# Performance work log

Hardware: AMD Instinct MI355X
Metric: run time of the kernel (lower is better)

## Reference

```python
import jax, jax.numpy as jnp
import numpy as np

# Dimensions (see shape_source)
L = 1024   # episode_len (memory slots)
B = 64     # batch (parallel envs)
K = 512    # key_size
V = 512    # value_size
H = 8      # num_head
MEMB = 256 # memory_state_embedding
SDIM = 512 # state_dim
HID = 512  # hidden width of all 2-layer encoders
RIMQ = 512 # rim_query_size
LAT = K - MEMB  # task_inference_latent dim


def setup_inputs() -> dict:
    key = jax.random.key(0)
    ks = jax.random.split(key, 16)
    w = lambda k, shape: (jax.random.normal(k, shape, jnp.float32) * 0.02)
    return {
        "state": jax.random.normal(ks[0], (B, SDIM), jnp.float32),
        "task_inference_latent": jax.random.normal(ks[1], (B, LAT), jnp.float32),
        "keys": jax.random.normal(ks[2], (L, B, K), jnp.float32),
        "vals": jax.random.normal(ks[3], (L, B, V), jnp.float32),
        "rpe_mod": jax.random.uniform(ks[4], (L, B, 1), jnp.float32),
        "step": jnp.maximum(jax.random.randint(ks[5], (B,), 0, L), 1),
        "W_state": w(ks[6], (SDIM, MEMB)), "b_state": jnp.zeros((MEMB,), jnp.float32),
        "Wcq1": w(ks[7], (K, HID)), "bcq1": jnp.zeros((HID,), jnp.float32),
        "Wcq2": w(ks[8], (HID, K)), "bcq2": jnp.zeros((K,), jnp.float32),
        "Wq": w(ks[9], (K, H * K)), "bq": jnp.zeros((H * K,), jnp.float32),
        "Wagg": w(ks[10], (H * V, V)), "bagg": jnp.zeros((V,), jnp.float32),
        "Wrk1": w(ks[11], (V, HID)), "brk1": jnp.zeros((HID,), jnp.float32),
        "Wrk2": w(ks[12], (HID, RIMQ)), "brk2": jnp.zeros((RIMQ,), jnp.float32),
        "Wrv1": w(ks[13], (V, HID)), "brv1": jnp.zeros((HID,), jnp.float32),
        "Wrv2": w(ks[14], (HID, V)), "brv2": jnp.zeros((V,), jnp.float32),
    }


def reference(state, task_inference_latent, keys, vals, rpe_mod, step,
              W_state, b_state, Wcq1, bcq1, Wcq2, bcq2, Wq, bq, Wagg, bagg,
              Wrk1, brk1, Wrk2, brk2, Wrv1, brv1, Wrv2, brv2):
    # DND.read (exploration branch), vectorized over the batch loop.
    se = state @ W_state + b_state                         # state_encoder: [B, MEMB]
    q = jnp.concatenate([se, task_inference_latent], -1)   # [B, K]
    # concat_query_encoder: stacked Linears with NO nonlinearity (faithful to source)
    q = (q @ Wcq1 + bcq1) @ Wcq2 + bcq2                    # [B, K]
    q = (q @ Wq + bq).reshape(B, H, K)                     # multi-head queries

    mk = keys * rpe_mod                                    # RPE-modulated keys [L, B, K]
    scores = jnp.einsum('lbk,bhk->blh', mk, q) / jnp.sqrt(jnp.float32(K))  # [B, L, H]
    valid = jnp.arange(L)[None, :] < step[:, None]         # [B, L] only slots < step[i]
    scores = jnp.where(valid[:, :, None], scores, jnp.float32(-1e30))
    prob = jax.nn.softmax(scores, axis=1) * valid[:, :, None].astype(scores.dtype)

    result = jnp.einsum('blh,lbv->bhv', prob, vals).reshape(B, H * V)
    result = (result @ Wagg + bagg)[:, None, :]            # value_aggregator -> [B, 1, V]
    out_key = (result @ Wrk1 + brk1) @ Wrk2 + brk2         # read_memory_to_key  [B, 1, RIMQ]
    out_val = (result @ Wrv1 + brv1) @ Wrv2 + brv2         # read_memory_to_value [B, 1, V]
    return out_key, out_val
```

## Files before the change

### kernel.cpp

```cpp
#include <hip/hip_runtime.h>
#include <math.h>

#define F4(p)  (*reinterpret_cast<float4*>(p))
#define CF4(p) (*reinterpret_cast<const float4*>(p))

#define NCHUNK 32

__device__ __forceinline__ void gemm_core(
    const float* __restrict__ Asrc, const float* __restrict__ inbias,
    const float* __restrict__ til,
    int NS, int srcld, int kc, int k0,
    const float* __restrict__ W, int ldw, int n0,
    const float* __restrict__ obias, float* __restrict__ Pout, int ldo)
{
    __shared__ float As[16*64], Ws[16*64];
    const int t = threadIdx.x;
    const int tx = t & 15, ty = t >> 4;
    const int row = t >> 2, kq = (t & 3) * 4;
    const int wrow = t >> 4, wcol = (t & 15) * 4;
    float acc[4][4] = {};
    for (int kk = 0; kk < kc; kk += 16) {
        const int kg = k0 + kk + kq;
        float4 av;
        if (til && kg >= 256) {
            av = CF4(&til[row*256 + (kg - 256)]);
        } else {
            av = {0.f, 0.f, 0.f, 0.f};
            if (inbias) av = CF4(&inbias[kg]);
            for (int s = 0; s < NS; ++s) {
                float4 v = CF4(&Asrc[(size_t)(s*64 + row)*srcld + kg]);
                av.x += v.x; av.y += v.y; av.z += v.z; av.w += v.w;
            }
        }
        As[(kq+0)*64+row] = av.x; As[(kq+1)*64+row] = av.y;
        As[(kq+2)*64+row] = av.z; As[(kq+3)*64+row] = av.w;
        F4(&Ws[wrow*64 + wcol]) = CF4(&W[(size_t)(k0 + kk + wrow)*ldw + n0 + wcol]);
        __syncthreads();
        #pragma unroll
        for (int k = 0; k < 16; ++k) {
            float4 a4 = CF4(&As[k*64 + ty*4]);
            float4 w4 = CF4(&Ws[k*64 + tx*4]);
            float a[4] = {a4.x, a4.y, a4.z, a4.w};
            float w[4] = {w4.x, w4.y, w4.z, w4.w};
            #pragma unroll
            for (int i = 0; i < 4; ++i)
                #pragma unroll
                for (int j = 0; j < 4; ++j)
                    acc[i][j] += a[i] * w[j];
        }
        __syncthreads();
    }
    #pragma unroll
    for (int i = 0; i < 4; ++i) {
        float4 o = {acc[i][0], acc[i][1], acc[i][2], acc[i][3]};
        if (obias) {
            float4 ob = CF4(&obias[n0 + tx*4]);
            o.x += ob.x; o.y += ob.y; o.z += ob.z; o.w += ob.w;
        }
        F4(&Pout[(size_t)(ty*4 + i)*ldo + n0 + tx*4]) = o;
    }
}

__global__ __launch_bounds__(256) void k_q1(
    const float* __restrict__ state, const float* __restrict__ W_state,
    float* __restrict__ P1)
{
    const int nt = blockIdx.x, ks = blockIdx.y;
    gemm_core(state, nullptr, nullptr, 1, 512, 64, ks*64,
              W_state, 256, nt*64, nullptr, P1 + (size_t)ks*64*256, 256);
}

__global__ __launch_bounds__(256) void k_q2(
    const float* __restrict__ P1, const float* __restrict__ b_state,
    const float* __restrict__ til, const float* __restrict__ Wcq1,
    float* __restrict__ P2)
{
    const int nt = blockIdx.x, ks = blockIdx.y;
    gemm_core(P1, b_state, til, 8, 256, 64, ks*64,
              Wcq1, 512, nt*64, nullptr, P2 + (size_t)ks*64*512, 512);
}

__global__ __launch_bounds__(256) void k_q3(
    const float* __restrict__ P2, const float* __restrict__ bcq1,
    const float* __restrict__ Wcq2, float* __restrict__ P3)
{
    const int nt = blockIdx.x, ks = blockIdx.y;
    gemm_core(P2, bcq1, nullptr, 8, 512, 64, ks*64,
              Wcq2, 512, nt*64, nullptr, P3 + (size_t)ks*64*512, 512);
}

__global__ __launch_bounds__(256) void k_qh(
    const float* __restrict__ P3, const float* __restrict__ bcq2,
    const float* __restrict__ Wq, float* __restrict__ P4)
{
    const int nt = blockIdx.x, ks = blockIdx.y;
    gemm_core(P3, bcq2, nullptr, 8, 512, 128, ks*128,
              Wq, 4096, nt*64, nullptr, P4 + (size_t)ks*64*4096, 4096);
}

__global__ __launch_bounds__(256) void k_qsum(
    const float* __restrict__ P4, const float* __restrict__ bq,
    float* __restrict__ qh)
{
    const int b = blockIdx.x, t = threadIdx.x;
    #pragma unroll
    for (int j = 0; j < 4; ++j) {
        int f = t + j*256;
        float4 v = CF4(&bq[f*4]);
        #pragma unroll
        for (int s = 0; s < 4; ++s) {
            float4 u = CF4(&P4[(size_t)(s*64 + b)*4096 + f*4]);
            v.x += u.x; v.y += u.y; v.z += u.z; v.w += u.w;
        }
        F4(&qh[(size_t)b*4096 + f*4]) = v;
    }
}

__global__ __launch_bounds__(256) void k_fa(
    const float* __restrict__ keys, const float* __restrict__ rpe,
    const float* __restrict__ qh, const float* __restrict__ vals,
    const int* __restrict__ step,
    float* __restrict__ Facc, float* __restrict__ Fms)
{
    __shared__ float s_q[4096];
    __shared__ float s_sc[64*8];
    __shared__ float red[256];
    __shared__ float s_m[8];
    const int b = blockIdx.y, lc = blockIdx.x;
    const int sb = step[b];
    const int l0 = (lc * sb) / NCHUNK;
    const int l1 = ((lc + 1) * sb) / NCHUNK;
    const int nl = l1 - l0;
    const int t = threadIdx.x;
    float* facc_out = Facc + ((size_t)(lc*64) + b)*4096;
    if (nl <= 0) {
        float4 z = {0.f, 0.f, 0.f, 0.f};
        for (int i = t; i < 1024; i += 256) F4(&facc_out[i*4]) = z;
        if (t < 8) {
            size_t o = ((size_t)(lc*64 + b)*8 + t)*2;
            Fms[o] = -1e30f; Fms[o+1] = 0.f;
        }
        return;
    }
    for (int i = t; i < 1024; i += 256)
        F4(&s_q[i*4]) = CF4(&qh[(size_t)b*4096 + i*4]);
    __syncthreads();
    const int lane = t & 63, w = t >> 6;
    float qr[8][8];
    #pragma unroll
    for (int h = 0; h < 8; ++h) {
        float4 x = CF4(&s_q[h*512 + lane*8]);
        float4 y = CF4(&s_q[h*512 + lane*8 + 4]);
        qr[h][0]=x.x; qr[h][1]=x.y; qr[h][2]=x.z; qr[h][3]=x.w;
        qr[h][4]=y.x; qr[h][5]=y.y; qr[h][6]=y.z; qr[h][7]=y.w;
    }
    const float inv_sqrtK = 0.04419417382415922f;
    const bool p0 = lane & 1, p1 = lane & 2, p2 = lane & 4;
    const size_t kstride = (size_t)4*64*512;
    const float* kp = keys + ((size_t)(l0 + w)*64 + b)*512 + lane*8;
    float4 k0x, k0y, k1x, k1y;
    if (w < nl)     { k0x = CF4(kp);           k0y = CF4(kp + 4); }
    if (w + 4 < nl) { k1x = CF4(kp + kstride); k1y = CF4(kp + kstride + 4); }
    for (int il = w; il < nl; il += 4) {
        float kv[8] = {k0x.x,k0x.y,k0x.z,k0x.w, k0y.x,k0y.y,k0y.z,k0y.w};
        k0x = k1x; k0y = k1y;
        if (il + 8 < nl) { k1x = CF4(kp + 2*kstride); k1y = CF4(kp + 2*kstride + 4); }
        kp += kstride;
        float pr[8] = {};
        #pragma unroll
        for (int h = 0; h < 8; ++h)
            #pragma unroll
            for (int j = 0; j < 8; ++j)
                pr[h] += kv[j] * qr[h][j];
        float w4[4], x2[2], y;
        #pragma unroll
        for (int i = 0; i < 4; ++i) {
            float keep = p0 ? pr[2*i+1] : pr[2*i];
            float send = p0 ? pr[2*i]   : pr[2*i+1];
            w4[i] = keep + __shfl_xor(send, 1);
        }
        #pragma unroll
        for (int i = 0; i < 2; ++i) {
            float keep = p1 ? w4[2*i+1] : w4[2*i];
            float send = p1 ? w4[2*i]   : w4[2*i+1];
            x2[i] = keep + __shfl_xor(send, 2);
        }
        {
            float keep = p2 ? x2[1] : x2[0];
            float send = p2 ? x2[0] : x2[1];
            y = keep + __shfl_xor(send, 4);
        }
        y += __shfl_xor(y, 8);
        y += __shfl_xor(y, 16);
        y += __shfl_xor(y, 32);
        if (lane < 8)
            s_sc[il*8 + lane] = y * rpe[(l0 + il)*64 + b] * inv_sqrtK;
    }
    __syncthreads();
    const int h = t & 7, g = t >> 3;
    float m = -1e30f;
    for (int l = g; l < nl; l += 32) m = fmaxf(m, s_sc[l*8 + h]);
    red[g*8 + h] = m;
    __syncthreads();
    #pragma unroll
    for (int s = 16; s; s >>= 1) {
        if (g < s) red[g*8+h] = fmaxf(red[g*8+h], red[(g+s)*8+h]);
        __syncthreads();
    }
    if (t < 8) s_m[t] = red[t];
    __syncthreads();
    float mh = s_m[h], s_acc = 0.f;
    for (int l = g; l < nl; l += 32) {
        float e = __expf(s_sc[l*8 + h] - mh);
        s_sc[l*8 + h] = e;
        s_acc += e;
    }
    red[g*8 + h] = s_acc;
    __syncthreads();
    #pragma unroll
    for (int s = 16; s; s >>= 1) {
        if (g < s) red[g*8+h] += red[(g+s)*8+h];
        __syncthreads();
    }
    if (t < 8) {
        size_t o = ((size_t)(lc*64 + b)*8 + t)*2;
        Fms[o] = s_m[t]; Fms[o+1] = red[t];
    }
    const int par = t >> 7, c = t & 127;
    float4 acc[8] = {};
    const size_t vstride = (size_t)2*64*512;
    const float* vp = vals + ((size_t)(l0 + par)*64 + b)*512 + c*4;
    float4 v0, v1, v2;
    if (par < nl)     v0 = CF4(vp);
    if (par + 2 < nl) v1 = CF4(vp + vstride);
    if (par + 4 < nl) v2 = CF4(vp + 2*vstride);
    for (int il = par; il < nl; il += 2) {
        float4 pa = CF4(&s_sc[il*8]);
        float4 pb = CF4(&s_sc[il*8 + 4]);
        acc[0].x += pa.x*v0.x; acc[0].y += pa.x*v0.y; acc[0].z += pa.x*v0.z; acc[0].w += pa.x*v0.w;
        acc[1].x += pa.y*v0.x; acc[1].y += pa.y*v0.y; acc[1].z += pa.y*v0.z; acc[1].w += pa.y*v0.w;
        acc[2].x += pa.z*v0.x; acc[2].y += pa.z*v0.y; acc[2].z += pa.z*v0.z; acc[2].w += pa.z*v0.w;
        acc[3].x += pa.w*v0.x; acc[3].y += pa.w*v0.y; acc[3].z += pa.w*v0.z; acc[3].w += pa.w*v0.w;
        acc[4].x += pb.x*v0.x; acc[4].y += pb.x*v0.y; acc[4].z += pb.x*v0.z; acc[4].w += pb.x*v0.w;
        acc[5].x += pb.y*v0.x; acc[5].y += pb.y*v0.y; acc[5].z += pb.y*v0.z; acc[5].w += pb.y*v0.w;
        acc[6].x += pb.z*v0.x; acc[6].y += pb.z*v0.y; acc[6].z += pb.z*v0.z; acc[6].w += pb.z*v0.w;
        acc[7].x += pb.w*v0.x; acc[7].y += pb.w*v0.y; acc[7].z += pb.w*v0.z; acc[7].w += pb.w*v0.w;
        v0 = v1; v1 = v2;
        if (il + 6 < nl) v2 = CF4(vp + 3*vstride);
        vp += vstride;
    }
    __syncthreads();
    if (par == 1) {
        #pragma unroll
        for (int hh = 0; hh < 8; ++hh)
            F4(&s_q[(c*8 + hh)*4]) = acc[hh];
    }
    __syncthreads();
    if (par == 0) {
        #pragma unroll
        for (int hh = 0; hh < 8; ++hh) {
            float4 o = CF4(&s_q[(c*8 + hh)*4]);
            o.x += acc[hh].x; o.y += acc[hh].y; o.z += acc[hh].z; o.w += acc[hh].w;
            F4(&facc_out[hh*512 + c*4]) = o;
        }
    }
}

__global__ __launch_bounds__(256) void k_comb(
    const float* __restrict__ Facc, const float* __restrict__ Fms,
    float* __restrict__ res)
{
    __shared__ float wgt[NCHUNK*8];
    const int b = blockIdx.x, t = threadIdx.x;
    if (t < 8) {
        float mm[NCHUNK], ss[NCHUNK], e[NCHUNK];
        float M = -1e30f;
        #pragma unroll
        for (int i = 0; i < NCHUNK; ++i) {
            size_t o = ((size_t)(i*64 + b)*8 + t)*2;
            mm[i] = Fms[o]; ss[i] = Fms[o+1];
            M = fmaxf(M, mm[i]);
        }
        float D = 0.f;
        #pragma unroll
        for (int i = 0; i < NCHUNK; ++i) { e[i] = __expf(mm[i] - M); D += e[i]*ss[i]; }
        float invD = 1.f / D;
        #pragma unroll
        for (int i = 0; i < NCHUNK; ++i) wgt[i*8 + t] = e[i] * invD;
    }
    __syncthreads();
    #pragma unroll
    for (int j = 0; j < 4; ++j) {
        int f = t + j*256;
        int h = f >> 7;
        float4 a = {0.f, 0.f, 0.f, 0.f};
        #pragma unroll
        for (int i = 0; i < NCHUNK; ++i) {
            float wi = wgt[i*8 + h];
            float4 v = CF4(&Facc[((size_t)(i*64) + b)*4096 + f*4]);
            a.x += wi*v.x; a.y += wi*v.y; a.z += wi*v.z; a.w += wi*v.w;
        }
        F4(&res[(size_t)b*4096 + f*4]) = a;
    }
}

__global__ __launch_bounds__(256) void k_agg(
    const float* __restrict__ res, const float* __restrict__ Wagg,
    float* __restrict__ P5)
{
    const int nt = blockIdx.x, ks = blockIdx.y;
    gemm_core(res, nullptr, nullptr, 1, 4096, 128, ks*128,
              Wagg, 512, nt*64, nullptr, P5 + (size_t)ks*64*512, 512);
}

__global__ __launch_bounds__(256) void k_rkv1(
    const float* __restrict__ P5, const float* __restrict__ bagg,
    const float* __restrict__ Wrk1, const float* __restrict__ Wrv1,
    float* __restrict__ P6)
{
    const int nt = blockIdx.x, ks = blockIdx.y, z = blockIdx.z;
    gemm_core(P5, bagg, nullptr, 32, 512, 128, ks*128,
              z ? Wrv1 : Wrk1, 512, nt*64,
              nullptr, P6 + (size_t)(z*4 + ks)*64*512, 512);
}

__global__ __launch_bounds__(256) void k_rkv2(
    const float* __restrict__ P6,
    const float* __restrict__ brk1, const float* __restrict__ brv1,
    const float* __restrict__ Wrk2, const float* __restrict__ Wrv2,
    const float* __restrict__ brk2, const float* __restrict__ brv2,
    float* __restrict__ out)
{
    const int nt = blockIdx.x, z = blockIdx.z;
    gemm_core(P6 + (size_t)z*4*64*512, z ? brv1 : brk1, nullptr, 4, 512, 512, 0,
              z ? Wrv2 : Wrk2, 512, nt*64,
              z ? brv2 : brk2, out + (size_t)z*64*512, 512);
}

extern "C" void kernel_launch(void* const* d_in, const int* in_sizes, int n_in,
                              void* d_out, int out_size, void* d_ws, size_t ws_size,
                              hipStream_t stream) {
    const float* state   = (const float*)d_in[0];
    const float* til     = (const float*)d_in[1];
    const float* keys    = (const float*)d_in[2];
    const float* vals    = (const float*)d_in[3];
    const float* rpe     = (const float*)d_in[4];
    const int*   step    = (const int*)d_in[5];
    const float* W_state = (const float*)d_in[6];
    const float* b_state = (const float*)d_in[7];
    const float* Wcq1 = (const float*)d_in[8];
    const float* bcq1 = (const float*)d_in[9];
    const float* Wcq2 = (const float*)d_in[10];
    const float* bcq2 = (const float*)d_in[11];
    const float* Wq   = (const float*)d_in[12];
    const float* bq   = (const float*)d_in[13];
    const float* Wagg = (const float*)d_in[14];
    const float* bagg = (const float*)d_in[15];
    const float* Wrk1 = (const float*)d_in[16];
    const float* brk1 = (const float*)d_in[17];
    const float* Wrk2 = (const float*)d_in[18];
    const float* brk2 = (const float*)d_in[19];
    const float* Wrv1 = (const float*)d_in[20];
    const float* brv1 = (const float*)d_in[21];
    const float* Wrv2 = (const float*)d_in[22];
    const float* brv2 = (const float*)d_in[23];
    float* out = (float*)d_out;
    float* ws  = (float*)d_ws;

    float* P1   = ws;
    float* P2   = ws + 131072;
    float* P3   = ws + 393216;
    float* P4   = ws + 655360;
    float* qh   = ws + 1703936;
    float* Facc = ws + 1966080;
    float* Fms  = ws + 10354688;
    float* res  = ws + 10387456;
    float* P5   = ws;
    float* P6   = ws + 1048576;

    k_q1  <<<dim3(4,8),   256, 0, stream>>>(state, W_state, P1);
    k_q2  <<<dim3(8,8),   256, 0, stream>>>(P1, b_state, til, Wcq1, P2);
    k_q3  <<<dim3(8,8),   256, 0, stream>>>(P2, bcq1, Wcq2, P3);
    k_qh  <<<dim3(64,4),  256, 0, stream>>>(P3, bcq2, Wq, P4);
    k_qsum<<<64, 256, 0, stream>>>(P4, bq, qh);
    k_fa  <<<dim3(NCHUNK,64), 256, 0, stream>>>(keys, rpe, qh, vals, step, Facc, Fms);
    k_comb<<<64, 256, 0, stream>>>(Facc, Fms, res);
    k_agg <<<dim3(8,32),  256, 0, stream>>>(res, Wagg, P5);
    k_rkv1<<<dim3(8,4,2), 256, 0, stream>>>(P5, bagg, Wrk1, Wrv1, P6);
    k_rkv2<<<dim3(8,1,2), 256, 0, stream>>>(P6, brk1, brv1, Wrk2, Wrv2,
                                            brk2, brv2, out);
}
```

Baseline: 169.4 us.

## Stage keys and values through double-buffered LDS tiles in attention kernel

The attention kernel now loads keys and values cooperatively, four rows at a time, into double-buffered shared-memory tiles with register prefetch. Queries are read from LDS inside the loop instead of being held in 64 registers per thread. This frees registers so launch_bounds can request 4 blocks per unit, and the chunk count is halved to 16 with workspace offsets adjusted to match. The trade is two barriers per tile, extra LDS traffic, and less L-parallelism per batch row.

```diff
diff --git a/kernel.cpp b/kernel.cpp
--- a/kernel.cpp
+++ b/kernel.cpp
@@ -4,7 +4,7 @@
 #define F4(p)  (*reinterpret_cast<float4*>(p))
 #define CF4(p) (*reinterpret_cast<const float4*>(p))
 
-#define NCHUNK 32
+#define NCHUNK 16
 
 __device__ __forceinline__ void gemm_core(
     const float* __restrict__ Asrc, const float* __restrict__ inbias,
@@ -116,14 +116,16 @@
     }
 }
 
-__global__ __launch_bounds__(256) void k_fa(
+__global__ __launch_bounds__(256, 4) void k_fa(
     const float* __restrict__ keys, const float* __restrict__ rpe,
     const float* __restrict__ qh, const float* __restrict__ vals,
     const int* __restrict__ step,
     float* __restrict__ Facc, float* __restrict__ Fms)
 {
     __shared__ float s_q[4096];
+    __shared__ float s_kt[2][2048];
     __shared__ float s_sc[64*8];
+    __shared__ float s_rpe[64];
     __shared__ float red[256];
     __shared__ float s_m[8];
     const int b = blockIdx.y, lc = blockIdx.x;
@@ -142,61 +144,80 @@
         }
         return;
     }
-    for (int i = t; i < 1024; i += 256)
-        F4(&s_q[i*4]) = CF4(&qh[(size_t)b*4096 + i*4]);
-    __syncthreads();
+    const int ntile = (nl + 3) >> 2;
+    const int j0 = t, j1 = t + 256;
+    const int r0 = j0 >> 7, c0 = (j0 & 127) * 4;
+    const int r1 = j1 >> 7, c1 = (j1 & 127) * 4;
+    const float inv_sqrtK = 0.04419417382415922f;
+
+    {
+        int la = min(l0 + r0, sb - 1), lb = min(l0 + r1, sb - 1);
+        float4 ra = CF4(&keys[((size_t)la*64 + b)*512 + c0]);
+        float4 rb = CF4(&keys[((size_t)lb*64 + b)*512 + c1]);
+        for (int i = t; i < 1024; i += 256)
+            F4(&s_q[i*4]) = CF4(&qh[(size_t)b*4096 + i*4]);
+        if (t < nl) s_rpe[t] = rpe[(l0 + t)*64 + b] * inv_sqrtK;
+        F4(&s_kt[0][j0*4]) = ra;
+        F4(&s_kt[0][j1*4]) = rb;
+    }
+    __syncthreads();
+
     const int lane = t & 63, w = t >> 6;
-    float qr[8][8];
-    #pragma unroll
-    for (int h = 0; h < 8; ++h) {
-        float4 x = CF4(&s_q[h*512 + lane*8]);
-        float4 y = CF4(&s_q[h*512 + lane*8 + 4]);
-        qr[h][0]=x.x; qr[h][1]=x.y; qr[h][2]=x.z; qr[h][3]=x.w;
-        qr[h][4]=y.x; qr[h][5]=y.y; qr[h][6]=y.z; qr[h][7]=y.w;
-    }
-    const float inv_sqrtK = 0.04419417382415922f;
     const bool p0 = lane & 1, p1 = lane & 2, p2 = lane & 4;
-    const size_t kstride = (size_t)4*64*512;
-    const float* kp = keys + ((size_t)(l0 + w)*64 + b)*512 + lane*8;
-    float4 k0x, k0y, k1x, k1y;
-    if (w < nl)     { k0x = CF4(kp);           k0y = CF4(kp + 4); }
-    if (w + 4 < nl) { k1x = CF4(kp + kstride); k1y = CF4(kp + kstride + 4); }
-    for (int il = w; il < nl; il += 4) {
-        float kv[8] = {k0x.x,k0x.y,k0x.z,k0x.w, k0y.x,k0y.y,k0y.z,k0y.w};
-        k0x = k1x; k0y = k1y;
-        if (il + 8 < nl) { k1x = CF4(kp + 2*kstride); k1y = CF4(kp + 2*kstride + 4); }
-        kp += kstride;
-        float pr[8] = {};
-        #pragma unroll
-        for (int h = 0; h < 8; ++h)
+    for (int i = 0; i < ntile; ++i) {
+        const int cur = i & 1;
+        float4 ra, rb;
+        const bool more = (i + 1 < ntile);
+        if (more) {
+            int la = min(l0 + (i+1)*4 + r0, sb - 1);
+            int lb = min(l0 + (i+1)*4 + r1, sb - 1);
+            ra = CF4(&keys[((size_t)la*64 + b)*512 + c0]);
+            rb = CF4(&keys[((size_t)lb*64 + b)*512 + c1]);
+        }
+        const int r = i*4 + w;
+        if (r < nl) {
+            float4 kx = CF4(&s_kt[cur][w*512 + lane*8]);
+            float4 ky = CF4(&s_kt[cur][w*512 + lane*8 + 4]);
+            float kv[8] = {kx.x,kx.y,kx.z,kx.w, ky.x,ky.y,ky.z,ky.w};
+            float pr[8] = {};
             #pragma unroll
-            for (int j = 0; j < 8; ++j)
-                pr[h] += kv[j] * qr[h][j];
-        float w4[4], x2[2], y;
-        #pragma unroll
-        for (int i = 0; i < 4; ++i) {
-            float keep = p0 ? pr[2*i+1] : pr[2*i];
-            float send = p0 ? pr[2*i]   : pr[2*i+1];
-            w4[i] = keep + __shfl_xor(send, 1);
-        }
-        #pragma unroll
-        for (int i = 0; i < 2; ++i) {
-            float keep = p1 ? w4[2*i+1] : w4[2*i];
-            float send = p1 ? w4[2*i]   : w4[2*i+1];
-            x2[i] = keep + __shfl_xor(send, 2);
-        }
-        {
-            float keep = p2 ? x2[1] : x2[0];
-            float send = p2 ? x2[0] : x2[1];
-            y = keep + __shfl_xor(send, 4);
-        }
-        y += __shfl_xor(y, 8);
-        y += __shfl_xor(y, 16);
-        y += __shfl_xor(y, 32);
-        if (lane < 8)
-            s_sc[il*8 + lane] = y * rpe[(l0 + il)*64 + b] * inv_sqrtK;
-    }
-    __syncthreads();
+            for (int h = 0; h < 8; ++h) {
+                float4 qx = CF4(&s_q[h*512 + lane*8]);
+                float4 qy = CF4(&s_q[h*512 + lane*8 + 4]);
+                pr[h] = kv[0]*qx.x + kv[1]*qx.y + kv[2]*qx.z + kv[3]*qx.w
+                      + kv[4]*qy.x + kv[5]*qy.y + kv[6]*qy.z + kv[7]*qy.w;
+            }
+            float w4[4], x2[2], y;
+            #pragma unroll
+            for (int q = 0; q < 4; ++q) {
+                float keep = p0 ? pr[2*q+1] : pr[2*q];
+                float send = p0 ? pr[2*q]   : pr[2*q+1];
+                w4[q] = keep + __shfl_xor(send, 1);
+            }
+            #pragma unroll
+            for (int q = 0; q < 2; ++q) {
+                float keep = p1 ? w4[2*q+1] : w4[2*q];
+                float send = p1 ? w4[2*q]   : w4[2*q+1];
+                x2[q] = keep + __shfl_xor(send, 2);
+            }
+            {
+                float keep = p2 ? x2[1] : x2[0];
+                float send = p2 ? x2[0] : x2[1];
+                y = keep + __shfl_xor(send, 4);
+            }
+            y += __shfl_xor(y, 8);
+            y += __shfl_xor(y, 16);
+            y += __shfl_xor(y, 32);
+            if (lane < 8)
+                s_sc[r*8 + lane] = y * s_rpe[r];
+        }
+        __syncthreads();
+        if (more) {
+            F4(&s_kt[cur ^ 1][j0*4]) = ra;
+            F4(&s_kt[cur ^ 1][j1*4]) = rb;
+        }
+        __syncthreads();
+    }
     const int h = t & 7, g = t >> 3;
     float m = -1e30f;
     for (int l = g; l < nl; l += 32) m = fmaxf(m, s_sc[l*8 + h]);
@@ -226,30 +247,52 @@
         size_t o = ((size_t)(lc*64 + b)*8 + t)*2;
         Fms[o] = s_m[t]; Fms[o+1] = red[t];
     }
+    __syncthreads();
     const int par = t >> 7, c = t & 127;
     float4 acc[8] = {};
-    const size_t vstride = (size_t)2*64*512;
-    const float* vp = vals + ((size_t)(l0 + par)*64 + b)*512 + c*4;
-    float4 v0, v1, v2;
-    if (par < nl)     v0 = CF4(vp);
-    if (par + 2 < nl) v1 = CF4(vp + vstride);
-    if (par + 4 < nl) v2 = CF4(vp + 2*vstride);
-    for (int il = par; il < nl; il += 2) {
-        float4 pa = CF4(&s_sc[il*8]);
-        float4 pb = CF4(&s_sc[il*8 + 4]);
-        acc[0].x += pa.x*v0.x; acc[0].y += pa.x*v0.y; acc[0].z += pa.x*v0.z; acc[0].w += pa.x*v0.w;
-        acc[1].x += pa.y*v0.x; acc[1].y += pa.y*v0.y; acc[1].z += pa.y*v0.z; acc[1].w += pa.y*v0.w;
-        acc[2].x += pa.z*v0.x; acc[2].y += pa.z*v0.y; acc[2].z += pa.z*v0.z; acc[2].w += pa.z*v0.w;
-        acc[3].x += pa.w*v0.x; acc[3].y += pa.w*v0.y; acc[3].z += pa.w*v0.z; acc[3].w += pa.w*v0.w;
-        acc[4].x += pb.x*v0.x; acc[4].y += pb.x*v0.y; acc[4].z += pb.x*v0.z; acc[4].w += pb.x*v0.w;
-        acc[5].x += pb.y*v0.x; acc[5].y += pb.y*v0.y; acc[5].z += pb.y*v0.z; acc[5].w += pb.y*v0.w;
-        acc[6].x += pb.z*v0.x; acc[6].y += pb.z*v0.y; acc[6].z += pb.z*v0.z; acc[6].w += pb.z*v0.w;
-        acc[7].x += pb.w*v0.x; acc[7].y += pb.w*v0.y; acc[7].z += pb.w*v0.z; acc[7].w += pb.w*v0.w;
-        v0 = v1; v1 = v2;
-        if (il + 6 < nl) v2 = CF4(vp + 3*vstride);
-        vp += vstride;
-    }
-    __syncthreads();
+    {
+        int la = min(l0 + r0, sb - 1), lb = min(l0 + r1, sb - 1);
+        float4 ra = CF4(&vals[((size_t)la*64 + b)*512 + c0]);
+        float4 rb = CF4(&vals[((size_t)lb*64 + b)*512 + c1]);
+        F4(&s_kt[0][j0*4]) = ra;
+        F4(&s_kt[0][j1*4]) = rb;
+    }
+    __syncthreads();
+    for (int i = 0; i < ntile; ++i) {
+        const int cur = i & 1;
+        float4 ra, rb;
+        const bool more = (i + 1 < ntile);
+        if (more) {
+            int la = min(l0 + (i+1)*4 + r0, sb - 1);
+            int lb = min(l0 + (i+1)*4 + r1, sb - 1);
+            ra = CF4(&vals[((size_t)la*64 + b)*512 + c0]);
+            rb = CF4(&vals[((size_t)lb*64 + b)*512 + c1]);
+        }
+        #pragma unroll
+        for (int sub = 0; sub < 2; ++sub) {
+            const int tr = par + sub*2;
+            const int row = i*4 + tr;
+            if (row < nl) {
+                float4 v = CF4(&s_kt[cur][tr*512 + c*4]);
+                float4 pa = CF4(&s_sc[row*8]);
+                float4 pb = CF4(&s_sc[row*8 + 4]);
+                acc[0].x += pa.x*v.x; acc[0].y += pa.x*v.y; acc[0].z += pa.x*v.z; acc[0].w += pa.x*v.w;
+                acc[1].x += pa.y*v.x; acc[1].y += pa.y*v.y; acc[1].z += pa.y*v.z; acc[1].w += pa.y*v.w;
+                acc[2].x += pa.z*v.x; acc[2].y += pa.z*v.y; acc[2].z += pa.z*v.z; acc[2].w += pa.z*v.w;
+                acc[3].x += pa.w*v.x; acc[3].y += pa.w*v.y; acc[3].z += pa.w*v.z; acc[3].w += pa.w*v.w;
+                acc[4].x += pb.x*v.x; acc[4].y += pb.x*v.y; acc[4].z += pb.x*v.z; acc[4].w += pb.x*v.w;
+                acc[5].x += pb.y*v.x; acc[5].y += pb.y*v.y; acc[5].z += pb.y*v.z; acc[5].w += pb.y*v.w;
+                acc[6].x += pb.z*v.x; acc[6].y += pb.z*v.y; acc[6].z += pb.z*v.z; acc[6].w += pb.z*v.w;
+                acc[7].x += pb.w*v.x; acc[7].y += pb.w*v.y; acc[7].z += pb.w*v.z; acc[7].w += pb.w*v.w;
+            }
+        }
+        __syncthreads();
+        if (more) {
+            F4(&s_kt[cur ^ 1][j0*4]) = ra;
+            F4(&s_kt[cur ^ 1][j1*4]) = rb;
+        }
+        __syncthreads();
+    }
     if (par == 1) {
         #pragma unroll
         for (int hh = 0; hh < 8; ++hh)
@@ -373,8 +416,8 @@
     float* P4   = ws + 655360;
     float* qh   = ws + 1703936;
     float* Facc = ws + 1966080;
-    float* Fms  = ws + 10354688;
-    float* res  = ws + 10387456;
+    float* Fms  = ws + 6160384;
+    float* res  = ws + 6176768;
     float* P5   = ws;
     float* P6   = ws + 1048576;
 
```

Measured after the change: 166.9 us. No clear change (-1.4%).

## Use fixed 32-row attention chunks and skip chunks beyond each batch's step

Applied to the files above, without the earlier changes.

The flash-attention split now gives each block a fixed 32-row chunk of memory slots instead of dividing step[b] into 32 variable-length pieces. Blocks whose chunk starts at or beyond step[b] return at once without writing zeros, and the combine kernel reads only the ceil(step/32) chunks that hold data, normalising at the end. This cuts the zero-fill writes and the combine traffic for short-step batches and makes per-block work uniform. It also sets launch_bounds occupancy to 4, which may limit registers in the attention kernel.

```diff
diff --git a/kernel.cpp b/kernel.cpp
--- a/kernel.cpp
+++ b/kernel.cpp
@@ -4,7 +4,8 @@
 #define F4(p)  (*reinterpret_cast<float4*>(p))
 #define CF4(p) (*reinterpret_cast<const float4*>(p))
 
-#define NCHUNK 32
+#define ROWS  32
+#define MAXC  32
 
 __device__ __forceinline__ void gemm_core(
     const float* __restrict__ Asrc, const float* __restrict__ inbias,
@@ -116,32 +117,24 @@
     }
 }
 
-__global__ __launch_bounds__(256) void k_fa(
+__global__ __launch_bounds__(256, 4) void k_fa(
     const float* __restrict__ keys, const float* __restrict__ rpe,
     const float* __restrict__ qh, const float* __restrict__ vals,
     const int* __restrict__ step,
     float* __restrict__ Facc, float* __restrict__ Fms)
 {
     __shared__ float s_q[4096];
-    __shared__ float s_sc[64*8];
+    __shared__ float s_sc[ROWS*8];
     __shared__ float red[256];
     __shared__ float s_m[8];
     const int b = blockIdx.y, lc = blockIdx.x;
     const int sb = step[b];
-    const int l0 = (lc * sb) / NCHUNK;
-    const int l1 = ((lc + 1) * sb) / NCHUNK;
-    const int nl = l1 - l0;
+    const int l0 = lc * ROWS;
+    if (l0 >= sb) return;
+    const int nl = min(ROWS, sb - l0);
     const int t = threadIdx.x;
     float* facc_out = Facc + ((size_t)(lc*64) + b)*4096;
-    if (nl <= 0) {
-        float4 z = {0.f, 0.f, 0.f, 0.f};
-        for (int i = t; i < 1024; i += 256) F4(&facc_out[i*4]) = z;
-        if (t < 8) {
-            size_t o = ((size_t)(lc*64 + b)*8 + t)*2;
-            Fms[o] = -1e30f; Fms[o+1] = 0.f;
-        }
-        return;
-    }
+
     for (int i = t; i < 1024; i += 256)
         F4(&s_q[i*4]) = CF4(&qh[(size_t)b*4096 + i*4]);
     __syncthreads();
@@ -268,25 +261,24 @@
 
 __global__ __launch_bounds__(256) void k_comb(
     const float* __restrict__ Facc, const float* __restrict__ Fms,
-    float* __restrict__ res)
-{
-    __shared__ float wgt[NCHUNK*8];
+    const int* __restrict__ step, float* __restrict__ res)
+{
+    __shared__ float wgt[MAXC*8];
+    __shared__ float s_inv[8];
     const int b = blockIdx.x, t = threadIdx.x;
+    const int nc = (step[b] + ROWS - 1) / ROWS;
     if (t < 8) {
-        float mm[NCHUNK], ss[NCHUNK], e[NCHUNK];
         float M = -1e30f;
-        #pragma unroll
-        for (int i = 0; i < NCHUNK; ++i) {
+        for (int i = 0; i < nc; ++i)
+            M = fmaxf(M, Fms[((size_t)(i*64 + b)*8 + t)*2]);
+        float D = 0.f;
+        for (int i = 0; i < nc; ++i) {
             size_t o = ((size_t)(i*64 + b)*8 + t)*2;
-            mm[i] = Fms[o]; ss[i] = Fms[o+1];
-            M = fmaxf(M, mm[i]);
-        }
-        float D = 0.f;
-        #pragma unroll
-        for (int i = 0; i < NCHUNK; ++i) { e[i] = __expf(mm[i] - M); D += e[i]*ss[i]; }
-        float invD = 1.f / D;
-        #pragma unroll
-        for (int i = 0; i < NCHUNK; ++i) wgt[i*8 + t] = e[i] * invD;
+            float e = __expf(Fms[o] - M);
+            wgt[i*8 + t] = e;
+            D += e * Fms[o+1];
+        }
+        s_inv[t] = 1.f / D;
     }
     __syncthreads();
     #pragma unroll
@@ -294,12 +286,13 @@
         int f = t + j*256;
         int h = f >> 7;
         float4 a = {0.f, 0.f, 0.f, 0.f};
-        #pragma unroll
-        for (int i = 0; i < NCHUNK; ++i) {
+        for (int i = 0; i < nc; ++i) {
             float wi = wgt[i*8 + h];
             float4 v = CF4(&Facc[((size_t)(i*64) + b)*4096 + f*4]);
             a.x += wi*v.x; a.y += wi*v.y; a.z += wi*v.z; a.w += wi*v.w;
         }
+        float inv = s_inv[h];
+        a.x *= inv; a.y *= inv; a.z *= inv; a.w *= inv;
         F4(&res[(size_t)b*4096 + f*4]) = a;
     }
 }
@@ -383,8 +376,8 @@
     k_q3  <<<dim3(8,8),   256, 0, stream>>>(P2, bcq1, Wcq2, P3);
     k_qh  <<<dim3(64,4),  256, 0, stream>>>(P3, bcq2, Wq, P4);
     k_qsum<<<64, 256, 0, stream>>>(P4, bq, qh);
-    k_fa  <<<dim3(NCHUNK,64), 256, 0, stream>>>(keys, rpe, qh, vals, step, Facc, Fms);
-    k_comb<<<64, 256, 0, stream>>>(Facc, Fms, res);
+    k_fa  <<<dim3(MAXC,64), 256, 0, stream>>>(keys, rpe, qh, vals, step, Facc, Fms);
+    k_comb<<<64, 256, 0, stream>>>(Facc, Fms, step, res);
     k_agg <<<dim3(8,32),  256, 0, stream>>>(res, Wagg, P5);
     k_rkv1<<<dim3(8,4,2), 256, 0, stream>>>(P5, bagg, Wrk1, Wrv1, P6);
     k_rkv2<<<dim3(8,1,2), 256, 0, stream>>>(P6, brk1, brv1, Wrk2, Wrv2,
```

After: 181.8 us. 1.07x slower.
